# Kernel optimization log

Hardware: AMD Instinct MI355X
Metric: run time of the kernel (lower is better)

Reference implementation:

```python
import jax, jax.numpy as jnp
import numpy as np

B, S, DIN, PPOS = 2, 128, 768, 256
DCAT = 2 * (DIN + PPOS)   # 2048, BiLSTM input dim
H = DCAT // 2             # 1024, LSTM hidden per direction
MAXLEN = 128              # position embedding table size


def _xavier(k, shape):
    lim = float(np.sqrt(6.0 / (shape[0] + shape[1])))
    return jax.random.uniform(k, shape, jnp.float32, -lim, lim)


def _lstm_u(k, shape):
    lim = float(1.0 / np.sqrt(H))
    return jax.random.uniform(k, shape, jnp.float32, -lim, lim)


def setup_inputs() -> dict:
    key = jax.random.key(0)
    ks = jax.random.split(key, 17)
    inp = {
        "input_embeddings": jax.random.normal(ks[0], (B, S, DIN), jnp.float32),
        "pos_emb": _xavier(ks[1], (MAXLEN, PPOS)),
    }
    i = 2
    for l in (0, 1):
        for d in ("f", "b"):
            inp[f"w_ih_l{l}_{d}"] = _lstm_u(ks[i], (4 * H, DCAT)); i += 1
            inp[f"b_ih_l{l}_{d}"] = _lstm_u(ks[i], (4 * H,)); i += 1
            inp[f"b_hh_l{l}_{d}"] = _lstm_u(ks[i], (4 * H,)); i += 1
    inp["fc_w"] = _lstm_u(ks[i], (1, 2 * H)); i += 1
    inp["fc_b"] = _lstm_u(ks[i], (1,))
    inp["convo_len"] = S
    return inp


def _lstm_dir(x, w_ih, b_ih, b_hh):
    # single timestep, h0=c0=0 -> recurrent term vanishes (grad wrt W_hh is 0)
    g = x @ w_ih.T + b_ih + b_hh            # [N, 4H], pytorch gate order i,f,g,o
    i, f, c, o = jnp.split(g, 4, axis=-1)
    cell = jax.nn.sigmoid(i) * jnp.tanh(c)  # f-gate multiplies c0=0
    return jax.nn.sigmoid(o) * jnp.tanh(cell)


def reference(input_embeddings, pos_emb,
              w_ih_l0_f, b_ih_l0_f, b_hh_l0_f,
              w_ih_l0_b, b_ih_l0_b, b_hh_l0_b,
              w_ih_l1_f, b_ih_l1_f, b_hh_l1_f,
              w_ih_l1_b, b_ih_l1_b, b_hh_l1_b,
              fc_w, fc_b, convo_len):
    # positions indexed by int(norm(embedding)) as in the original code
    idx = jnp.linalg.norm(input_embeddings, axis=-1).astype(jnp.int32)  # [B,S]
    e = jnp.concatenate([input_embeddings, pos_emb[idx]], axis=-1)      # [B,S,D']
    # pair (i,j) -> concat(e_i, e_j)
    left = jnp.repeat(e, S, axis=1)          # [B, S*S, D'], row i repeated S times
    right = jnp.tile(e, (1, S, 1))           # [B, S*S, D'], sequence tiled S times
    p = jnp.concatenate([left, right], axis=-1).reshape(B * S * S, DCAT)
    h1 = jnp.concatenate([
        _lstm_dir(p, w_ih_l0_f, b_ih_l0_f, b_hh_l0_f),
        _lstm_dir(p, w_ih_l0_b, b_ih_l0_b, b_hh_l0_b)], axis=-1)        # [N, 2H]
    h2 = jnp.concatenate([
        _lstm_dir(h1, w_ih_l1_f, b_ih_l1_f, b_hh_l1_f),
        _lstm_dir(h1, w_ih_l1_b, b_ih_l1_b, b_hh_l1_b)], axis=-1)       # [N, 2H]
    logits = h2 @ fc_w.T + fc_b              # [N, 1]
    return logits.reshape(B, S * S)
```

## Files before the change

### kernel.cpp

```cpp
#include <hip/hip_runtime.h>
#include <cstdint>

typedef _Float16 f16;
typedef f16   f16x8 __attribute__((ext_vector_type(8)));
typedef f16   f16x4 __attribute__((ext_vector_type(4)));
typedef float f32x4 __attribute__((ext_vector_type(4)));
typedef float f32x8 __attribute__((ext_vector_type(8)));
typedef int   i32x4 __attribute__((ext_vector_type(4)));
typedef signed char c8x8 __attribute__((ext_vector_type(8)));
typedef unsigned int u32;


static constexpr size_t OFF_E16  = 0;
static constexpr size_t OFF_W0P  = 524288;
static constexpr size_t OFF_UV   = 34078720;
static constexpr size_t OFF_B0   = 50855936;
static constexpr size_t OFF_W1P  = 50888704;
static constexpr size_t OFF_B1   = 76054528;
static constexpr size_t OFF_H1   = 76079104;
static constexpr size_t OFF_PART = 210296832;

__device__ __forceinline__ void gl_lds16(const void* g, void* l) {
  __builtin_amdgcn_global_load_lds((const __attribute__((address_space(1))) u32*)g,
                                   (__attribute__((address_space(3))) u32*)l, 16, 0, 0);
}
__device__ __forceinline__ float sigm(float x) { return 1.f / (1.f + __expf(-x)); }
__device__ __forceinline__ float tanh_f(float x) {
  float e = __expf(-2.f * fabsf(x));
  float t = (1.f - e) / (1.f + e);
  return x < 0.f ? -t : t;
}


__global__ __launch_bounds__(256) void prep_e(const float* __restrict__ x,
                                              const float* __restrict__ pos,
                                              f16* __restrict__ e16) {
  int row = blockIdx.x;
  const float* xr = x + (size_t)row * 768;
  double ss = 0.0;
  for (int i = threadIdx.x; i < 768; i += 256) { float v = xr[i]; ss += (double)v * v; }
  __shared__ double red[256];
  red[threadIdx.x] = ss;
  __syncthreads();
  for (int s2 = 128; s2 > 0; s2 >>= 1) {
    if (threadIdx.x < s2) red[threadIdx.x] += red[threadIdx.x + s2];
    __syncthreads();
  }
  __shared__ int idx_s;
  if (threadIdx.x == 0) {
    int idx = (int)((float)sqrt(red[0]));
    idx_s = idx < 0 ? 0 : (idx > 127 ? 127 : idx);
  }
  __syncthreads();
  int idx = idx_s;
  for (int i = threadIdx.x; i < 1024; i += 256) {
    float v = (i < 768) ? xr[i] : pos[idx * 256 + (i - 768)];
    e16[(size_t)row * 1024 + i] = (f16)v;
  }
}

__global__ __launch_bounds__(256) void prep_w0(const float* __restrict__ w0f,
                                               const float* __restrict__ w0b,
                                               f16* __restrict__ w0p) {
  int t = blockIdx.x * 256 + threadIdx.x;
  int n = t >> 8;
  int k4 = (t & 255) * 4;
  int half = n >> 13;
  int nn = n & 8191;
  int d = nn >> 12;
  int r = nn & 4095;
  const float* w = d ? w0b : w0f;
  float4 v = *(const float4*)(w + (size_t)r * 2048 + half * 1024 + k4);
  f16x4 o;
  o[0] = (f16)v.x; o[1] = (f16)v.y; o[2] = (f16)v.z; o[3] = (f16)v.w;
  *(f16x4*)(w0p + (size_t)n * 1024 + k4) = o;
}

__global__ __launch_bounds__(256) void prep_w1(const float* __restrict__ w1f,
                                               const float* __restrict__ w1b,
                                               signed char* __restrict__ w1q) {
  int t = blockIdx.x * 256 + threadIdx.x;
  int n = t >> 8;
  int c8 = (t & 255) * 8;
  int ct = n / 192, r = n % 192;
  int wn = r / 48, r2 = r % 48;
  int g = r2 >> 4, hs = r2 & 15;
  int d = ct >> 4;
  int h = (ct & 15) * 64 + wn * 16 + hs;
  int gsel = (g == 0) ? 0 : (g + 1);
  const float* w = d ? w1b : w1f;
  const float* src = w + (size_t)(gsel * 1024 + h) * 2048 + c8;
  float4 v0 = *(const float4*)(src);
  float4 v1 = *(const float4*)(src + 4);
  c8x8 o;
  o[0] = (signed char)(int)rintf(v0.x * 4064.f);
  o[1] = (signed char)(int)rintf(v0.y * 4064.f);
  o[2] = (signed char)(int)rintf(v0.z * 4064.f);
  o[3] = (signed char)(int)rintf(v0.w * 4064.f);
  o[4] = (signed char)(int)rintf(v1.x * 4064.f);
  o[5] = (signed char)(int)rintf(v1.y * 4064.f);
  o[6] = (signed char)(int)rintf(v1.z * 4064.f);
  o[7] = (signed char)(int)rintf(v1.w * 4064.f);
  *(c8x8*)(w1q + (size_t)n * 2048 + c8) = o;
}

__global__ void prep_bias(const float* bi0f, const float* bh0f,
                          const float* bi0b, const float* bh0b,
                          const float* bi1f, const float* bh1f,
                          const float* bi1b, const float* bh1b,
                          float* bias0, float* bias1) {
  int i = blockIdx.x * 256 + threadIdx.x;
  if (i < 8192) {
    int d = i >> 12, r = i & 4095;
    bias0[i] = d ? (bi0b[r] + bh0b[r]) : (bi0f[r] + bh0f[r]);
  } else if (i < 8192 + 6144) {
    int n = i - 8192;
    int d = n / 3072, rem = n % 3072;
    int g3 = rem >> 10, k = rem & 1023;
    int gsel = (g3 == 0) ? 0 : (g3 + 1);
    int r = gsel * 1024 + k;
    bias1[n] = d ? (bi1b[r] + bh1b[r]) : (bi1f[r] + bh1f[r]);
  }
}

__global__ __launch_bounds__(256) void gemm_l0(const f16* __restrict__ e16,
                                               const f16* __restrict__ w0p,
                                               float* __restrict__ uv) {
  __shared__ __align__(16) f16 As[8192];
  __shared__ __align__(16) f16 Bs[8192];
  int n0 = blockIdx.x * 128;
  int m0 = blockIdx.y * 128;
  int tid = threadIdx.x, lane = tid & 63, w = tid >> 6;
  int wr = (w >> 1) * 64, wc = (w & 1) * 64;
  f32x4 acc[4][4] = {};

  for (int k0 = 0; k0 < 1024; k0 += 64) {
    __syncthreads();
#pragma unroll
    for (int q = 0; q < 4; q++) {
      int ch = tid + q * 256;
      int c = ch >> 7, r = ch & 127;
      gl_lds16(e16 + (size_t)(m0 + r) * 1024 + k0 + c * 8, (char*)As + ch * 16);
    }
#pragma unroll
    for (int q = 0; q < 4; q++) {
      int ch = tid + q * 256;
      int c = ch >> 7, r = ch & 127;
      gl_lds16(w0p + (size_t)(n0 + r) * 1024 + k0 + c * 8, (char*)Bs + ch * 16);
    }
    __syncthreads();
#pragma unroll
    for (int ks = 0; ks < 2; ks++) {
      int cb = ks * 4 + (lane >> 4);
      f16x8 a[4], b[4];
#pragma unroll
      for (int f = 0; f < 4; f++)
        a[f] = *(const f16x8*)(As + (cb * 128 + wr + f * 16 + (lane & 15)) * 8);
#pragma unroll
      for (int g = 0; g < 4; g++)
        b[g] = *(const f16x8*)(Bs + (cb * 128 + wc + g * 16 + (lane & 15)) * 8);
#pragma unroll
      for (int f = 0; f < 4; f++)
#pragma unroll
        for (int g = 0; g < 4; g++)
          acc[f][g] = __builtin_amdgcn_mfma_f32_16x16x32_f16(a[f], b[g], acc[f][g], 0, 0, 0);
    }
  }
  int col = lane & 15, lg = lane >> 4;
#pragma unroll
  for (int f = 0; f < 4; f++)
#pragma unroll
    for (int g = 0; g < 4; g++)
#pragma unroll
      for (int j = 0; j < 4; j++) {
        int row = m0 + wr + f * 16 + lg * 4 + j;
        int c = n0 + wc + g * 16 + col;
        uv[(size_t)row * 16384 + c] = acc[f][g][j];
      }
}

__global__ __launch_bounds__(256) void pair_h1(const float* __restrict__ uv,
                                               const float* __restrict__ bias0,
                                               signed char* __restrict__ h1q) {
  int row = blockIdx.x;
  int urow = row >> 7;
  int b = row >> 14;
  int vrow = (b << 7) | (row & 127);
  int t = threadIdx.x;
  int u = t * 8;
  int d = u >> 10, k = u & 1023;
  const float* ub = uv + (size_t)urow * 16384 + d * 4096 + k;
  const float* vb = uv + (size_t)vrow * 16384 + 8192 + d * 4096 + k;
  const float* bb = bias0 + d * 4096 + k;
  f32x8 ui = *(const f32x8*)(ub);
  f32x8 uc = *(const f32x8*)(ub + 2048);
  f32x8 uo = *(const f32x8*)(ub + 3072);
  f32x8 vi = *(const f32x8*)(vb);
  f32x8 vc = *(const f32x8*)(vb + 2048);
  f32x8 vo = *(const f32x8*)(vb + 3072);
  f32x8 bi = *(const f32x8*)(bb);
  f32x8 bc = *(const f32x8*)(bb + 2048);
  f32x8 bo = *(const f32x8*)(bb + 3072);
  c8x8 ov;
#pragma unroll
  for (int e = 0; e < 8; e++) {
    float gi = ui[e] + vi[e] + bi[e];
    float gc = uc[e] + vc[e] + bc[e];
    float go = uo[e] + vo[e] + bo[e];
    float cell = sigm(gi) * tanh_f(gc);
    float hv = sigm(go) * tanh_f(cell);
    ov[e] = (signed char)(int)rintf(hv * 127.f);
  }
  *(c8x8*)(h1q + (size_t)row * 2048 + u) = ov;
}

__global__ __launch_bounds__(256, 3) void gemm_l1(const signed char* __restrict__ h1q,
                                                  const signed char* __restrict__ w1q,
                                                  const float* __restrict__ bias1,
                                                  const float* __restrict__ fcw,
                                                  float* __restrict__ partial) {
  __shared__ __align__(16) signed char As[2][8192];
  __shared__ __align__(16) signed char Bs[3][12288];
  int ct = blockIdx.x;
  int m0 = blockIdx.y * 128;
  int d = ct >> 4;
  int tid = threadIdx.x, lane = tid & 63;
  int wn = tid >> 6;
  int la = lane & 15, lq = lane >> 4;
  int lh = la >> 1, lb = la & 1;
  int sA = (lb * 4 + lq) ^ lh;

  const signed char* asrc[2]; signed char* adst[2];
#pragma unroll
  for (int q = 0; q < 2; q++) {
    int ch = tid + q * 256, L = ch >> 3, s = ch & 7;
    int e = s ^ (L & 7), R = 2 * L + (e >> 2), c = e & 3;
    asrc[q] = h1q + (size_t)(m0 + R) * 2048 + c * 16;
    adst[q] = &As[0][ch * 16];
  }
  const signed char* bsrc[3]; signed char* bdst[3];
#pragma unroll
  for (int q = 0; q < 3; q++) {
    int ch = tid + q * 256, L = ch >> 3, s = ch & 7;
    int e = s ^ (L & 7), P = 2 * L + (e >> 2), c = e & 3;
    bsrc[q] = w1q + (size_t)(ct * 192 + P) * 2048 + c * 16;
    bdst[q] = &Bs[0][ch * 16];
  }
  auto stageA = [&](int t, int buf) {
#pragma unroll
    for (int q = 0; q < 2; q++) gl_lds16(asrc[q] + t * 64, adst[q] + buf * 8192);
  };
  auto stageB = [&](int t, int buf) {
#pragma unroll
    for (int q = 0; q < 3; q++) gl_lds16(bsrc[q] + t * 64, bdst[q] + buf * 12288);
  };

  i32x4 acc[8][3] = {};
  stageA(0, 0); stageB(0, 0); stageB(1, 1);
  asm volatile("s_waitcnt vmcnt(3)" ::: "memory");
  __builtin_amdgcn_s_barrier();

  int ab = 0, bb = 0;
  for (int t = 0; t < 32; ++t) {
    const signed char* Ab = &As[ab][0];
    const signed char* Bb = &Bs[bb][0];
    i32x4 af[8], bf[3];
#pragma unroll
    for (int rf = 0; rf < 8; rf++)
      af[rf] = *(const i32x4*)(Ab + ((rf * 8 + lh) * 8 + sA) * 16);
#pragma unroll
    for (int cf = 0; cf < 3; cf++)
      bf[cf] = *(const i32x4*)(Bb + ((wn * 24 + cf * 8 + lh) * 8 + sA) * 16);
    if (t < 31) stageA(t + 1, ab ^ 1);
    if (t < 30) stageB(t + 2, bb == 0 ? 2 : bb - 1);
    __builtin_amdgcn_s_setprio(1);
#pragma unroll
    for (int rf = 0; rf < 8; rf++)
#pragma unroll
      for (int cf = 0; cf < 3; cf++)
        acc[rf][cf] = __builtin_amdgcn_mfma_i32_16x16x64_i8(af[rf], bf[cf], acc[rf][cf], 0, 0, 0);
    __builtin_amdgcn_s_setprio(0);
    if (t < 30)      { asm volatile("s_waitcnt vmcnt(3)" ::: "memory"); }
    else             { asm volatile("s_waitcnt vmcnt(0)" ::: "memory"); }
    __builtin_amdgcn_sched_barrier(0);
    __builtin_amdgcn_s_barrier();
    ab ^= 1; bb = (bb == 2) ? 0 : bb + 1;
  }

  float* sred = (float*)&As[0][0];
  const float S = 1.0f / 516128.0f;
  int hcol = (ct & 15) * 64 + wn * 16 + la;
  float bi = bias1[(d * 3 + 0) * 1024 + hcol];
  float bc = bias1[(d * 3 + 1) * 1024 + hcol];
  float bo = bias1[(d * 3 + 2) * 1024 + hcol];
  float wf = fcw[d * 1024 + hcol];
#pragma unroll
  for (int rf = 0; rf < 8; rf++) {
#pragma unroll
    for (int j = 0; j < 4; j++) {
      float gi = (float)acc[rf][0][j] * S + bi;
      float gc = (float)acc[rf][1][j] * S + bc;
      float go = (float)acc[rf][2][j] * S + bo;
      float cell = sigm(gi) * tanh_f(gc);
      float hv = sigm(go) * tanh_f(cell);
      float v = hv * wf;
      v += __shfl_xor(v, 1);
      v += __shfl_xor(v, 2);
      v += __shfl_xor(v, 4);
      v += __shfl_xor(v, 8);
      if (la == 0) sred[wn * 128 + rf * 16 + lq * 4 + j] = v;
    }
  }
  __syncthreads();
  if (tid < 128) {
    float s = sred[tid] + sred[128 + tid] + sred[256 + tid] + sred[384 + tid];
    partial[(size_t)ct * 32768 + m0 + tid] = s;
  }
}

__global__ void reduce_out(const float* __restrict__ partial,
                           const float* __restrict__ fcb,
                           float* __restrict__ out) {
  int m = blockIdx.x * 256 + threadIdx.x;
  float s = fcb[0];
#pragma unroll
  for (int ct = 0; ct < 32; ct++) s += partial[(size_t)ct * 32768 + m];
  out[m] = s;
}

extern "C" void kernel_launch(void* const* d_in, const int* in_sizes, int n_in,
                              void* d_out, int out_size, void* d_ws, size_t ws_size,
                              hipStream_t stream) {
  const float* x    = (const float*)d_in[0];
  const float* pos  = (const float*)d_in[1];
  const float* w0f  = (const float*)d_in[2];
  const float* bi0f = (const float*)d_in[3];
  const float* bh0f = (const float*)d_in[4];
  const float* w0b  = (const float*)d_in[5];
  const float* bi0b = (const float*)d_in[6];
  const float* bh0b = (const float*)d_in[7];
  const float* w1f  = (const float*)d_in[8];
  const float* bi1f = (const float*)d_in[9];
  const float* bh1f = (const float*)d_in[10];
  const float* w1b  = (const float*)d_in[11];
  const float* bi1b = (const float*)d_in[12];
  const float* bh1b = (const float*)d_in[13];
  const float* fcw  = (const float*)d_in[14];
  const float* fcb  = (const float*)d_in[15];
  float* out = (float*)d_out;

  char* ws = (char*)d_ws;
  f16*   e16   = (f16*)(ws + OFF_E16);
  f16*   w0p   = (f16*)(ws + OFF_W0P);
  float* uv    = (float*)(ws + OFF_UV);
  float* bias0 = (float*)(ws + OFF_B0);
  signed char* w1q = (signed char*)(ws + OFF_W1P);
  float* bias1 = (float*)(ws + OFF_B1);
  signed char* h1q = (signed char*)(ws + OFF_H1);
  float* part  = (float*)(ws + OFF_PART);

  prep_e<<<256, 256, 0, stream>>>(x, pos, e16);
  prep_w0<<<16384, 256, 0, stream>>>(w0f, w0b, w0p);
  prep_w1<<<6144, 256, 0, stream>>>(w1f, w1b, w1q);
  prep_bias<<<56, 256, 0, stream>>>(bi0f, bh0f, bi0b, bh0b, bi1f, bh1f, bi1b, bh1b,
                                    bias0, bias1);
  gemm_l0<<<dim3(128, 2), 256, 0, stream>>>(e16, w0p, uv);
  pair_h1<<<32768, 256, 0, stream>>>(uv, bias0, h1q);
  gemm_l1<<<dim3(32, 256), 256, 0, stream>>>(h1q, w1q, bias1, fcw, part);
  reduce_out<<<128, 256, 0, stream>>>(part, fcb, out);
}
```

Measured before the change: 699.9 us.

## Switch layer-1 int8 GEMM to 32x32x32 MFMA with 2x2 wave tiling

Rewrites the layer-1 int8 GEMM inner loop to use the 32x32x32 i8 MFMA instead of 16x16x64, with waves tiled 2x2 over rows and gate columns instead of each wave covering all 128 rows. The weight prep permutation is changed to match the new column grouping, and the epilogue reduction is adapted to the 32x32 accumulator layout. The aim is fewer LDS fragment reads per MFMA and higher MFMA throughput. The new lane-to-row mapping in the epilogue and the LDS swizzle offsets must match exactly, or results will be wrong.

```diff
diff --git a/kernel.cpp b/kernel.cpp
--- a/kernel.cpp
+++ b/kernel.cpp
@@ -7,6 +7,7 @@
 typedef float f32x4 __attribute__((ext_vector_type(4)));
 typedef float f32x8 __attribute__((ext_vector_type(8)));
 typedef int   i32x4 __attribute__((ext_vector_type(4)));
+typedef int   i32x16 __attribute__((ext_vector_type(16)));
 typedef signed char c8x8 __attribute__((ext_vector_type(8)));
 typedef unsigned int u32;
 
@@ -83,10 +84,10 @@
   int n = t >> 8;
   int c8 = (t & 255) * 8;
   int ct = n / 192, r = n % 192;
-  int wn = r / 48, r2 = r % 48;
-  int g = r2 >> 4, hs = r2 & 15;
+  int wc = r / 96, r2 = r % 96;
+  int g = r2 >> 5, q = r2 & 31;
   int d = ct >> 4;
-  int h = (ct & 15) * 64 + wn * 16 + hs;
+  int h = (ct & 15) * 64 + wc * 32 + q;
   int gsel = (g == 0) ? 0 : (g + 1);
   const float* w = d ? w1b : w1f;
   const float* src = w + (size_t)(gsel * 1024 + h) * 2048 + c8;
@@ -224,11 +225,9 @@
   int ct = blockIdx.x;
   int m0 = blockIdx.y * 128;
   int d = ct >> 4;
-  int tid = threadIdx.x, lane = tid & 63;
-  int wn = tid >> 6;
-  int la = lane & 15, lq = lane >> 4;
-  int lh = la >> 1, lb = la & 1;
-  int sA = (lb * 4 + lq) ^ lh;
+  int tid = threadIdx.x, lane = tid & 63, w = tid >> 6;
+  int wm = w >> 1, wc = w & 1;
+  int l31 = lane & 31, hi5 = lane >> 5, lp = lane & 1, lh2 = l31 >> 1;
 
   const signed char* asrc[2]; signed char* adst[2];
 #pragma unroll
@@ -255,7 +254,14 @@
     for (int q = 0; q < 3; q++) gl_lds16(bsrc[q] + t * 64, bdst[q] + buf * 12288);
   };
 
-  i32x4 acc[8][3] = {};
+  int s0 = ((lp << 2) | hi5) ^ (lh2 & 7);
+  int s1 = ((lp << 2) | (2 + hi5)) ^ (lh2 & 7);
+  int aoff0 = ((wm * 32 + lh2) * 8 + s0) * 16;
+  int aoff1 = ((wm * 32 + lh2) * 8 + s1) * 16;
+  int boff0 = ((wc * 48 + lh2) * 8 + s0) * 16;
+  int boff1 = ((wc * 48 + lh2) * 8 + s1) * 16;
+
+  i32x16 acc[2][3] = {};
   stageA(0, 0); stageB(0, 0); stageB(1, 1);
   asm volatile("s_waitcnt vmcnt(3)" ::: "memory");
   __builtin_amdgcn_s_barrier();
@@ -264,21 +270,27 @@
   for (int t = 0; t < 32; ++t) {
     const signed char* Ab = &As[ab][0];
     const signed char* Bb = &Bs[bb][0];
-    i32x4 af[8], bf[3];
-#pragma unroll
-    for (int rf = 0; rf < 8; rf++)
-      af[rf] = *(const i32x4*)(Ab + ((rf * 8 + lh) * 8 + sA) * 16);
-#pragma unroll
-    for (int cf = 0; cf < 3; cf++)
-      bf[cf] = *(const i32x4*)(Bb + ((wn * 24 + cf * 8 + lh) * 8 + sA) * 16);
+    i32x4 af[2][2], bf[2][3];
+#pragma unroll
+    for (int rf = 0; rf < 2; rf++) {
+      af[0][rf] = *(const i32x4*)(Ab + aoff0 + rf * 2048);
+      af[1][rf] = *(const i32x4*)(Ab + aoff1 + rf * 2048);
+    }
+#pragma unroll
+    for (int g = 0; g < 3; g++) {
+      bf[0][g] = *(const i32x4*)(Bb + boff0 + g * 2048);
+      bf[1][g] = *(const i32x4*)(Bb + boff1 + g * 2048);
+    }
     if (t < 31) stageA(t + 1, ab ^ 1);
     if (t < 30) stageB(t + 2, bb == 0 ? 2 : bb - 1);
     __builtin_amdgcn_s_setprio(1);
 #pragma unroll
-    for (int rf = 0; rf < 8; rf++)
-#pragma unroll
-      for (int cf = 0; cf < 3; cf++)
-        acc[rf][cf] = __builtin_amdgcn_mfma_i32_16x16x64_i8(af[rf], bf[cf], acc[rf][cf], 0, 0, 0);
+    for (int ks = 0; ks < 2; ks++)
+#pragma unroll
+      for (int rf = 0; rf < 2; rf++)
+#pragma unroll
+        for (int g = 0; g < 3; g++)
+          acc[rf][g] = __builtin_amdgcn_mfma_i32_32x32x32_i8(af[ks][rf], bf[ks][g], acc[rf][g], 0, 0, 0);
     __builtin_amdgcn_s_setprio(0);
     if (t < 30)      { asm volatile("s_waitcnt vmcnt(3)" ::: "memory"); }
     else             { asm volatile("s_waitcnt vmcnt(0)" ::: "memory"); }
@@ -289,18 +301,18 @@
 
   float* sred = (float*)&As[0][0];
   const float S = 1.0f / 516128.0f;
-  int hcol = (ct & 15) * 64 + wn * 16 + la;
+  int hcol = (ct & 15) * 64 + wc * 32 + l31;
   float bi = bias1[(d * 3 + 0) * 1024 + hcol];
   float bc = bias1[(d * 3 + 1) * 1024 + hcol];
   float bo = bias1[(d * 3 + 2) * 1024 + hcol];
   float wf = fcw[d * 1024 + hcol];
 #pragma unroll
-  for (int rf = 0; rf < 8; rf++) {
-#pragma unroll
-    for (int j = 0; j < 4; j++) {
-      float gi = (float)acc[rf][0][j] * S + bi;
-      float gc = (float)acc[rf][1][j] * S + bc;
-      float go = (float)acc[rf][2][j] * S + bo;
+  for (int rf = 0; rf < 2; rf++) {
+#pragma unroll
+    for (int reg = 0; reg < 16; reg++) {
+      float gi = (float)acc[rf][0][reg] * S + bi;
+      float gc = (float)acc[rf][1][reg] * S + bc;
+      float go = (float)acc[rf][2][reg] * S + bo;
       float cell = sigm(gi) * tanh_f(gc);
       float hv = sigm(go) * tanh_f(cell);
       float v = hv * wf;
@@ -308,12 +320,16 @@
       v += __shfl_xor(v, 2);
       v += __shfl_xor(v, 4);
       v += __shfl_xor(v, 8);
-      if (la == 0) sred[wn * 128 + rf * 16 + lq * 4 + j] = v;
+      v += __shfl_xor(v, 16);
+      if (l31 == 0) {
+        int row = wm * 64 + rf * 32 + (reg & 3) + 8 * (reg >> 2) + 4 * hi5;
+        sred[wc * 128 + row] = v;
+      }
     }
   }
   __syncthreads();
   if (tid < 128) {
-    float s = sred[tid] + sred[128 + tid] + sred[256 + tid] + sred[384 + tid];
+    float s = sred[tid] + sred[128 + tid];
     partial[(size_t)ct * 32768 + m0 + tid] = s;
   }
 }
```

Result: slower. 764.2 us (+9.2%).
